# Kernel optimization log

Hardware: AMD Instinct MI355X
Metric: run time of the kernel (lower is better)

## Reference

```python
import jax, jax.numpy as jnp
import numpy as np

B, T, D, H = 8, 2048, 512, 128

def setup_inputs() -> dict:
    key = jax.random.key(0)
    ks = jax.random.split(key, 8)
    s = lambda fan_in: 1.0 / np.sqrt(fan_in)
    return {
        "x": jax.random.normal(ks[0], (B, T, D), jnp.float32),
        "prediction": jax.random.normal(ks[1], (B, T, D), jnp.float32),
        "Wq": jax.random.uniform(ks[2], (D, H), jnp.float32, -s(D), s(D)),
        "bq": jnp.zeros((H,), jnp.float32),
        "Wk": jax.random.uniform(ks[3], (D, H), jnp.float32, -s(D), s(D)),
        "bk": jnp.zeros((H,), jnp.float32),
        "Wv": jax.random.uniform(ks[4], (D, D), jnp.float32, -s(D), s(D)),
        "bv": jnp.zeros((D,), jnp.float32),
        "Wf": jax.random.uniform(ks[5], (2 * D, D), jnp.float32, -s(2 * D), s(2 * D)),
        "bf": jnp.zeros((D,), jnp.float32),
    }

def reference(x, prediction, Wq, bq, Wk, bk, Wv, bv, Wf, bf):
    # q,k: [B,T,H]; v: [B,T,D]
    q = jnp.einsum('btd,dh->bth', prediction, Wq) + bq
    k = jnp.einsum('btd,dh->bth', x, Wk) + bk
    v = jnp.einsum('btd,de->bte', x, Wv) + bv
    # unscaled attention scores [B,T,T]
    scores = jnp.einsum('bth,bsh->bts', q, k)
    attn = jax.nn.softmax(scores, axis=-1)
    attended = jnp.einsum('bts,bsd->btd', attn, v)
    fusion_input = jnp.concatenate([prediction, attended], axis=-1)  # [B,T,2D]
    return jax.nn.sigmoid(jnp.einsum('btf,fd->btd', fusion_input, Wf) + bf)
```

## Files before the change

### kernel.cpp

```cpp
#include <hip/hip_runtime.h>
#include <hip/hip_bf16.h>


#define APF_B 8
#define APF_T 2048
#define APF_D 512
#define APF_H 128
#define APF_M (APF_B * APF_T)
#define FA_SB 128

typedef unsigned short u16;
typedef __attribute__((ext_vector_type(8))) short short8;
typedef __attribute__((ext_vector_type(4))) float f32x4;
typedef __attribute__((ext_vector_type(16))) float f32x16;

static __device__ __forceinline__ u16 f2bf(float x) {
    union { float f; unsigned int u; } cv;
    cv.f = x;
    unsigned int u = cv.u + 0x7FFFu + ((cv.u >> 16) & 1u);
    return (u16)(u >> 16);
}

static __device__ __forceinline__ void load16_lds(const u16* g, u16* l) {
    __builtin_amdgcn_global_load_lds(
        (const __attribute__((address_space(1))) unsigned int*)g,
        (__attribute__((address_space(3))) unsigned int*)l,
        16, 0, 0);
}

static __device__ __forceinline__ f32x16 zero16() {
    f32x16 v;
#pragma unroll
    for (int i = 0; i < 16; ++i) v[i] = 0.f;
    return v;
}


__global__ __launch_bounds__(256) void cvt_pair(const float* __restrict__ in0,
                                                u16* __restrict__ out0,
                                                const float* __restrict__ in1,
                                                u16* __restrict__ out1, long n4)
{
    long i = blockIdx.x * 256L + threadIdx.x;
    const long stride = (long)gridDim.x * 256L;
    for (; i < 2 * n4; i += stride) {
        const float* in = (i < n4) ? in0 : in1;
        u16* out = (i < n4) ? out0 : out1;
        const long j = (i < n4) ? i : (i - n4);
        const float4 v = ((const float4*)in)[j];
        ushort4 o;
        o.x = f2bf(v.x); o.y = f2bf(v.y); o.z = f2bf(v.z); o.w = f2bf(v.w);
        ((ushort4*)out)[j] = o;
    }
}

__global__ __launch_bounds__(256) void prep_weights(
    const float* __restrict__ Wq, u16* __restrict__ WqT,
    const float* __restrict__ Wk, u16* __restrict__ WkT,
    const float* __restrict__ Wv, u16* __restrict__ WvT,
    const float* __restrict__ Wf, u16* __restrict__ WfT)
{
    const long e = blockIdx.x * 256L + threadIdx.x;
    if (e < 65536) {
        const long idx = e;
        const long n = idx / 512, k = idx % 512;
        WqT[idx] = f2bf(Wq[k * 128 + n]);
    } else if (e < 131072) {
        const long idx = e - 65536;
        const long n = idx / 512, k = idx % 512;
        WkT[idx] = f2bf(Wk[k * 128 + n]);
    } else if (e < 393216) {
        const long idx = e - 131072;
        const long n = idx / 512, k = idx % 512;
        WvT[idx] = f2bf(Wv[k * 512 + n]);
    } else if (e < 917504) {
        const long idx = e - 393216;
        const long n = idx / 1024, k = idx % 1024;
        WfT[idx] = f2bf(Wf[k * 512 + n]);
    }
}

template <int DUAL, int EPI, int BIASM, int VBLK>
__global__ __launch_bounds__(256) void mfma_gemm(
    const u16* __restrict__ Ap, const u16* __restrict__ A2p, long lda,
    const u16* __restrict__ Bp, const u16* __restrict__ Bp2, long ldb,
    const float* __restrict__ biasp, const float* __restrict__ bias2,
    void* __restrict__ Cp, void* __restrict__ Cp2, long ldc, int K,
    long sA, long sB, long sC)
{
    __shared__ u16 smA[128 * 32];
    __shared__ u16 smB[128 * 32];

    const int tid  = threadIdx.x;
    const int lane = tid & 63;
    const int wid  = tid >> 6;
    const int wr   = wid >> 1;
    const int wc   = wid & 1;

    const long row0 = (long)blockIdx.y * 128;
    const long col0 = (long)blockIdx.x * 128;
    const long z    = blockIdx.z;

    const u16* Abase = (DUAL == 2) ? (z ? A2p : Ap) : (Ap + z * sA);
    const u16* Bbase = (DUAL == 2) ? (z ? Bp2 : Bp) : (Bp + z * sB);

    f32x4 acc[4][4];
#pragma unroll
    for (int i = 0; i < 4; ++i)
#pragma unroll
        for (int j = 0; j < 4; ++j)
            acc[i][j] = (f32x4){0.f, 0.f, 0.f, 0.f};

    const int lrow = (lane >> 4) * 4;
    const int lcol = lane & 15;
    const int q8   = (lane >> 4) * 8;

    for (int kb = 0; kb < K; kb += 32) {
#pragma unroll
        for (int rep = 0; rep < 2; ++rep) {
            const int c  = tid + rep * 256;
            const int r  = c >> 2;
            const int kc = (c & 3) * 8;
            const int wbase = (wid * 64 + rep * 256) * 8;
            const u16* ga;
            if (DUAL == 1 && (kb + kc) >= APF_D) {
                ga = A2p + (row0 + r) * lda + (kb + kc - APF_D);
            } else {
                ga = Abase + (row0 + r) * lda + (kb + kc);
            }
            load16_lds(ga, &smA[wbase]);
            const u16* gb = Bbase + (col0 + r) * ldb + (kb + kc);
            load16_lds(gb, &smB[wbase]);
        }
        __syncthreads();

        short8 av[4], bv4[4];
#pragma unroll
        for (int ti = 0; ti < 4; ++ti)
            av[ti] = *(const short8*)&smA[(wr * 64 + ti * 16 + lcol) * 32 + q8];
#pragma unroll
        for (int tj = 0; tj < 4; ++tj)
            bv4[tj] = *(const short8*)&smB[(wc * 64 + tj * 16 + lcol) * 32 + q8];

#pragma unroll
        for (int ti = 0; ti < 4; ++ti)
#pragma unroll
            for (int tj = 0; tj < 4; ++tj)
                acc[ti][tj] = __builtin_amdgcn_mfma_f32_16x16x32_bf16(
                    av[ti], bv4[tj], acc[ti][tj], 0, 0, 0);
        __syncthreads();
    }

    const float* bias = (DUAL == 2 && z) ? bias2 : biasp;

#pragma unroll
    for (int ti = 0; ti < 4; ++ti) {
        const long m0t = row0 + wr * 64 + ti * 16 + lrow;
#pragma unroll
        for (int tj = 0; tj < 4; ++tj) {
            const long n = col0 + wc * 64 + tj * 16 + lcol;
            const float bn = (BIASM == 0 && bias != nullptr) ? bias[n] : 0.f;
            if (EPI == 0) {
                u16* C = (u16*)((DUAL == 2 && z) ? Cp2 : Cp) + ((DUAL == 2) ? 0 : z * sC);
#pragma unroll
                for (int r = 0; r < 4; ++r) {
                    const long m = m0t + r;
                    const float bm = (BIASM == 1) ? bias[m] : bn;
                    long idx;
                    if (VBLK) {
                        idx = ((((m >> 5) * 256) + (n >> 3)) << 8) +
                              ((m & 31) << 3) + (n & 7);
                    } else {
                        idx = m * ldc + n;
                    }
                    C[idx] = f2bf(acc[ti][tj][r] + bm);
                }
            } else {
                float* C = (float*)Cp;
#pragma unroll
                for (int r = 0; r < 4; ++r) {
                    const float val = acc[ti][tj][r] + bn;
                    C[(m0t + r) * ldc + n] = 1.0f / (1.0f + expf(-val));
                }
            }
        }
    }
}

__global__ __launch_bounds__(256, 2) void attn_fused(
    const u16* __restrict__ qg, const u16* __restrict__ kg,
    const u16* __restrict__ vTg, u16* __restrict__ attg)
{
    __shared__ u16 sQ[64 * 128];
    __shared__ u16 sK[128 * 128];
    __shared__ u16 sP[64 * 128];
    __shared__ float sRSp[256];

    const int tid  = threadIdx.x;
    const int lane = tid & 63;
    const int w    = tid >> 6;
    const int l31  = lane & 31;
    const int hi   = lane >> 5;

    const int  bid = blockIdx.x;
    const long z   = bid & 7;
    const int  r   = bid >> 3;
    const long q0  = (long)(r & 31) * 64;
    const long d0  = (long)(r >> 5) * 256;

    const u16* kbase0 = kg + z * (long)APF_T * APF_H;

    {
        const u16* qsrc = qg + (z * APF_T + q0) * APF_H;
#pragma unroll
        for (int rep = 0; rep < 4; ++rep) {
            const int c    = tid + rep * 256;
            const int row  = c >> 4;
            const int col8 = (c & 15) * 8;
            load16_lds(qsrc + row * APF_H + (col8 ^ ((row & 7) << 3)), &sQ[c * 8]);
        }
#pragma unroll
        for (int rep = 0; rep < 8; ++rep) {
            const int c    = tid + rep * 256;
            const int row  = c >> 4;
            const int col8 = (c & 15) * 8;
            load16_lds(kbase0 + row * APF_H + (col8 ^ ((row & 7) << 3)), &sK[c * 8]);
        }
    }
    __syncthreads();

    f32x16 oacc[2][2];
#pragma unroll
    for (int i = 0; i < 2; ++i)
#pragma unroll
        for (int j = 0; j < 2; ++j) oacc[i][j] = zero16();
    f32x16 rsacc[2];
    rsacc[0] = zero16(); rsacc[1] = zero16();

    const long dblk0 = (d0 >> 5) + w * 2;
    const u16* vzb = vTg + z * 1048576L + dblk0 * 65536L + (long)l31 * 8;

    const int pcol = w * 32 + l31;
    const int krow = w * 32 + l31;

    for (int kt = 0; kt < APF_T / FA_SB; ++kt) {
        f32x16 sacc[2];
        sacc[0] = zero16(); sacc[1] = zero16();
#pragma unroll
        for (int ks = 0; ks < 8; ++ks) {
            const int colk = ks * 16 + hi * 8;
            const short8 bv = *(const short8*)&sK[krow * 128 + (colk ^ ((krow & 7) << 3))];
#pragma unroll
            for (int qt = 0; qt < 2; ++qt) {
                const int qrow = qt * 32 + l31;
                const short8 av = *(const short8*)&sQ[qrow * 128 + (colk ^ ((qrow & 7) << 3))];
                sacc[qt] = __builtin_amdgcn_mfma_f32_32x32x16_bf16(av, bv, sacc[qt], 0, 0, 0);
            }
        }
        __syncthreads();

        if (kt + 1 < APF_T / FA_SB) {
            const u16* ksrc = kbase0 + (long)(kt + 1) * FA_SB * APF_H;
#pragma unroll
            for (int rep = 0; rep < 8; ++rep) {
                const int c    = tid + rep * 256;
                const int row  = c >> 4;
                const int col8 = (c & 15) * 8;
                load16_lds(ksrc + row * APF_H + (col8 ^ ((row & 7) << 3)), &sK[c * 8]);
            }
        }

        const long sbase = (long)kt * 16 + hi;
        short8 vf1[2][4];
#pragma unroll
        for (int dt = 0; dt < 2; ++dt)
#pragma unroll
            for (int ks = 0; ks < 4; ++ks)
                vf1[dt][ks] = *(const short8*)(vzb + dt * 65536L + (sbase + ks * 2) * 256);

#pragma unroll
        for (int qt = 0; qt < 2; ++qt)
#pragma unroll
            for (int rg = 0; rg < 16; ++rg) {
                const float e = __expf(sacc[qt][rg]);
                rsacc[qt][rg] += e;
                const int prow = qt * 32 + (rg & 3) + 8 * (rg >> 2) + 4 * hi;
                sP[prow * 128 + (pcol ^ ((prow & 7) << 3))] = f2bf(e);
            }
        __syncthreads();

#pragma unroll
        for (int ks = 0; ks < 4; ++ks) {
            const int colk = ks * 16 + hi * 8;
            short8 pa[2];
#pragma unroll
            for (int qt = 0; qt < 2; ++qt) {
                const int prow = qt * 32 + l31;
                pa[qt] = *(const short8*)&sP[prow * 128 + (colk ^ ((prow & 7) << 3))];
            }
#pragma unroll
            for (int dt = 0; dt < 2; ++dt)
#pragma unroll
                for (int qt = 0; qt < 2; ++qt)
                    oacc[qt][dt] = __builtin_amdgcn_mfma_f32_32x32x16_bf16(
                        pa[qt], vf1[dt][ks], oacc[qt][dt], 0, 0, 0);
        }

        short8 vf2[2][4];
#pragma unroll
        for (int dt = 0; dt < 2; ++dt)
#pragma unroll
            for (int ks = 0; ks < 4; ++ks)
                vf2[dt][ks] = *(const short8*)(vzb + dt * 65536L + (sbase + 8 + ks * 2) * 256);

#pragma unroll
        for (int ks = 0; ks < 4; ++ks) {
            const int colk = (ks + 4) * 16 + hi * 8;
            short8 pa[2];
#pragma unroll
            for (int qt = 0; qt < 2; ++qt) {
                const int prow = qt * 32 + l31;
                pa[qt] = *(const short8*)&sP[prow * 128 + (colk ^ ((prow & 7) << 3))];
            }
#pragma unroll
            for (int dt = 0; dt < 2; ++dt)
#pragma unroll
                for (int qt = 0; qt < 2; ++qt)
                    oacc[qt][dt] = __builtin_amdgcn_mfma_f32_32x32x16_bf16(
                        pa[qt], vf2[dt][ks], oacc[qt][dt], 0, 0, 0);
        }
    }

#pragma unroll
    for (int qt = 0; qt < 2; ++qt)
#pragma unroll
        for (int rg = 0; rg < 16; ++rg) {
            float s = rsacc[qt][rg];
            s += __shfl_xor(s, 1);
            s += __shfl_xor(s, 2);
            s += __shfl_xor(s, 4);
            s += __shfl_xor(s, 8);
            s += __shfl_xor(s, 16);
            rsacc[qt][rg] = s;
        }
    if (l31 == 0) {
#pragma unroll
        for (int qt = 0; qt < 2; ++qt)
#pragma unroll
            for (int rg = 0; rg < 16; ++rg) {
                const int row = qt * 32 + (rg & 3) + 8 * (rg >> 2) + 4 * hi;
                sRSp[w * 64 + row] = rsacc[qt][rg];
            }
    }
    __syncthreads();
    if (tid < 64) {
        const float t = sRSp[tid] + sRSp[64 + tid] + sRSp[128 + tid] + sRSp[192 + tid];
        sRSp[tid] = 1.0f / t;
    }
    __syncthreads();

    const long rowg0 = z * APF_T + q0;
    const long colg0 = d0 + (long)w * 64;
#pragma unroll
    for (int qt = 0; qt < 2; ++qt)
#pragma unroll
        for (int rg = 0; rg < 16; ++rg) {
            const int row = qt * 32 + (rg & 3) + 8 * (rg >> 2) + 4 * hi;
            const float inv = sRSp[row];
#pragma unroll
            for (int dt = 0; dt < 2; ++dt)
                attg[(rowg0 + row) * APF_D + colg0 + dt * 32 + l31] =
                    f2bf(oacc[qt][dt][rg] * inv);
        }
}

extern "C" void kernel_launch(void* const* d_in, const int* in_sizes, int n_in,
                              void* d_out, int out_size, void* d_ws, size_t ws_size,
                              hipStream_t stream)
{
    (void)in_sizes; (void)n_in; (void)out_size; (void)ws_size;

    const float* x    = (const float*)d_in[0];
    const float* pred = (const float*)d_in[1];
    const float* Wq   = (const float*)d_in[2];
    const float* bq   = (const float*)d_in[3];
    const float* Wk   = (const float*)d_in[4];
    const float* bk   = (const float*)d_in[5];
    const float* Wv   = (const float*)d_in[6];
    const float* bv   = (const float*)d_in[7];
    const float* Wf   = (const float*)d_in[8];
    const float* bfu  = (const float*)d_in[9];

    u16* wsp   = (u16*)d_ws;
    u16* xb    = wsp;
    u16* predb = xb    + (long)APF_M * APF_D;
    u16* qb    = predb + (long)APF_M * APF_D;
    u16* kbuf  = qb    + (long)APF_M * APF_H;
    u16* vTb   = kbuf  + (long)APF_M * APF_H;
    u16* attb  = vTb   + (long)APF_M * APF_D;
    u16* WqT   = attb  + (long)APF_M * APF_D;
    u16* WkT   = WqT   + (long)APF_H * APF_D;
    u16* WvT   = WkT   + (long)APF_H * APF_D;
    u16* WfT   = WvT   + (long)APF_D * APF_D;

    const dim3 thr(256);
    const long nBTD4 = (long)APF_M * APF_D / 4;

    cvt_pair<<<dim3(1024), thr, 0, stream>>>(x, xb, pred, predb, nBTD4);
    prep_weights<<<dim3(3584), thr, 0, stream>>>(Wq, WqT, Wk, WkT, Wv, WvT, Wf, WfT);

    mfma_gemm<2, 0, 0, 0><<<dim3(1, 128, 2), thr, 0, stream>>>(
        predb, xb, APF_D, WqT, WkT, APF_D, bq, bk, qb, kbuf, APF_H, APF_D,
        0, 0, 0);

    mfma_gemm<0, 0, 1, 1><<<dim3(16, 4, 8), thr, 0, stream>>>(
        WvT, nullptr, APF_D, xb, nullptr, APF_D, bv, nullptr, vTb, nullptr,
        APF_T, APF_D, 0, (long)APF_T * APF_D, (long)APF_D * APF_T);

    attn_fused<<<dim3(512), thr, 0, stream>>>(qb, kbuf, vTb, attb);

    mfma_gemm<1, 2, 0, 0><<<dim3(4, 128, 1), thr, 0, stream>>>(
        predb, attb, APF_D, WfT, nullptr, 2 * APF_D, bfu, nullptr, d_out, nullptr,
        APF_D, 2 * APF_D, 0, 0, 0);
}
```

Before: 270.2 us.

## Merge prep kernels, double-buffer GEMM LDS, shrink attention key block

Fuses the input conversion and weight transpose into a single launch to remove one kernel launch. Adds double-buffered LDS staging in the MFMA GEMM so the next K-tile loads while the current one computes. Reworks the attention kernel to use 64-key blocks with the four waves split across query and key halves, cutting LDS use so three blocks can fit per CU, at the cost of more iterations and barriers. The GEMM overlap relies on the barrier at the end of each iteration and on the async LDS loads for the next tile finishing before that tile is read.

```diff
diff --git a/kernel.cpp b/kernel.cpp
--- a/kernel.cpp
+++ b/kernel.cpp
@@ -7,7 +7,7 @@
 #define APF_D 512
 #define APF_H 128
 #define APF_M (APF_B * APF_T)
-#define FA_SB 128
+#define FA_SB 64
 
 typedef unsigned short u16;
 typedef __attribute__((ext_vector_type(8))) short short8;
@@ -36,47 +36,46 @@
 }
 
 
-__global__ __launch_bounds__(256) void cvt_pair(const float* __restrict__ in0,
-                                                u16* __restrict__ out0,
-                                                const float* __restrict__ in1,
-                                                u16* __restrict__ out1, long n4)
-{
-    long i = blockIdx.x * 256L + threadIdx.x;
-    const long stride = (long)gridDim.x * 256L;
-    for (; i < 2 * n4; i += stride) {
-        const float* in = (i < n4) ? in0 : in1;
-        u16* out = (i < n4) ? out0 : out1;
-        const long j = (i < n4) ? i : (i - n4);
-        const float4 v = ((const float4*)in)[j];
-        ushort4 o;
-        o.x = f2bf(v.x); o.y = f2bf(v.y); o.z = f2bf(v.z); o.w = f2bf(v.w);
-        ((ushort4*)out)[j] = o;
-    }
-}
-
-__global__ __launch_bounds__(256) void prep_weights(
+__global__ __launch_bounds__(256) void prep_all(
+    const float* __restrict__ x,    u16* __restrict__ xb,
+    const float* __restrict__ pred, u16* __restrict__ predb, long n4,
     const float* __restrict__ Wq, u16* __restrict__ WqT,
     const float* __restrict__ Wk, u16* __restrict__ WkT,
     const float* __restrict__ Wv, u16* __restrict__ WvT,
     const float* __restrict__ Wf, u16* __restrict__ WfT)
 {
-    const long e = blockIdx.x * 256L + threadIdx.x;
-    if (e < 65536) {
-        const long idx = e;
-        const long n = idx / 512, k = idx % 512;
-        WqT[idx] = f2bf(Wq[k * 128 + n]);
-    } else if (e < 131072) {
-        const long idx = e - 65536;
-        const long n = idx / 512, k = idx % 512;
-        WkT[idx] = f2bf(Wk[k * 128 + n]);
-    } else if (e < 393216) {
-        const long idx = e - 131072;
-        const long n = idx / 512, k = idx % 512;
-        WvT[idx] = f2bf(Wv[k * 512 + n]);
-    } else if (e < 917504) {
-        const long idx = e - 393216;
-        const long n = idx / 1024, k = idx % 1024;
-        WfT[idx] = f2bf(Wf[k * 512 + n]);
+    const int bid = blockIdx.x;
+    if (bid < 1024) {
+        long i = bid * 256L + threadIdx.x;
+        const long stride = 1024 * 256L;
+        for (; i < 2 * n4; i += stride) {
+            const float* in = (i < n4) ? x : pred;
+            u16* out = (i < n4) ? xb : predb;
+            const long j = (i < n4) ? i : (i - n4);
+            const float4 v = ((const float4*)in)[j];
+            ushort4 o;
+            o.x = f2bf(v.x); o.y = f2bf(v.y); o.z = f2bf(v.z); o.w = f2bf(v.w);
+            ((ushort4*)out)[j] = o;
+        }
+    } else {
+        const long e = (bid - 1024) * 256L + threadIdx.x;
+        if (e < 65536) {
+            const long idx = e;
+            const long n = idx / 512, k = idx % 512;
+            WqT[idx] = f2bf(Wq[k * 128 + n]);
+        } else if (e < 131072) {
+            const long idx = e - 65536;
+            const long n = idx / 512, k = idx % 512;
+            WkT[idx] = f2bf(Wk[k * 128 + n]);
+        } else if (e < 393216) {
+            const long idx = e - 131072;
+            const long n = idx / 512, k = idx % 512;
+            WvT[idx] = f2bf(Wv[k * 512 + n]);
+        } else if (e < 917504) {
+            const long idx = e - 393216;
+            const long n = idx / 1024, k = idx % 1024;
+            WfT[idx] = f2bf(Wf[k * 512 + n]);
+        }
     }
 }
 
@@ -88,8 +87,8 @@
     void* __restrict__ Cp, void* __restrict__ Cp2, long ldc, int K,
     long sA, long sB, long sC)
 {
-    __shared__ u16 smA[128 * 32];
-    __shared__ u16 smB[128 * 32];
+    __shared__ u16 smA[2][128 * 32];
+    __shared__ u16 smB[2][128 * 32];
 
     const int tid  = threadIdx.x;
     const int lane = tid & 63;
@@ -115,7 +114,7 @@
     const int lcol = lane & 15;
     const int q8   = (lane >> 4) * 8;
 
-    for (int kb = 0; kb < K; kb += 32) {
+    auto stage = [&](int buf, int kb) {
 #pragma unroll
         for (int rep = 0; rep < 2; ++rep) {
             const int c  = tid + rep * 256;
@@ -128,19 +127,27 @@
             } else {
                 ga = Abase + (row0 + r) * lda + (kb + kc);
             }
-            load16_lds(ga, &smA[wbase]);
+            load16_lds(ga, &smA[buf][wbase]);
             const u16* gb = Bbase + (col0 + r) * ldb + (kb + kc);
-            load16_lds(gb, &smB[wbase]);
-        }
-        __syncthreads();
+            load16_lds(gb, &smB[buf][wbase]);
+        }
+    };
+
+    const int NT = K / 32;
+    stage(0, 0);
+    __syncthreads();
+    int cur = 0;
+
+    for (int t = 0; t < NT; ++t) {
+        if (t + 1 < NT) stage(cur ^ 1, (t + 1) * 32);
 
         short8 av[4], bv4[4];
 #pragma unroll
         for (int ti = 0; ti < 4; ++ti)
-            av[ti] = *(const short8*)&smA[(wr * 64 + ti * 16 + lcol) * 32 + q8];
+            av[ti] = *(const short8*)&smA[cur][(wr * 64 + ti * 16 + lcol) * 32 + q8];
 #pragma unroll
         for (int tj = 0; tj < 4; ++tj)
-            bv4[tj] = *(const short8*)&smB[(wc * 64 + tj * 16 + lcol) * 32 + q8];
+            bv4[tj] = *(const short8*)&smB[cur][(wc * 64 + tj * 16 + lcol) * 32 + q8];
 
 #pragma unroll
         for (int ti = 0; ti < 4; ++ti)
@@ -148,7 +155,9 @@
             for (int tj = 0; tj < 4; ++tj)
                 acc[ti][tj] = __builtin_amdgcn_mfma_f32_16x16x32_bf16(
                     av[ti], bv4[tj], acc[ti][tj], 0, 0, 0);
+
         __syncthreads();
+        cur ^= 1;
     }
 
     const float* bias = (DUAL == 2 && z) ? bias2 : biasp;
@@ -187,20 +196,22 @@
     }
 }
 
-__global__ __launch_bounds__(256, 2) void attn_fused(
+__global__ __launch_bounds__(256, 3) void attn_fused(
     const u16* __restrict__ qg, const u16* __restrict__ kg,
     const u16* __restrict__ vTg, u16* __restrict__ attg)
 {
     __shared__ u16 sQ[64 * 128];
-    __shared__ u16 sK[128 * 128];
-    __shared__ u16 sP[64 * 128];
-    __shared__ float sRSp[256];
+    __shared__ u16 sK[64 * 128];
+    __shared__ u16 sP[64 * 64];
+    __shared__ float sRS[192];
 
     const int tid  = threadIdx.x;
     const int lane = tid & 63;
     const int w    = tid >> 6;
     const int l31  = lane & 31;
     const int hi   = lane >> 5;
+    const int qb   = w >> 1;
+    const int sb   = w & 1;
 
     const int  bid = blockIdx.x;
     const long z   = bid & 7;
@@ -217,14 +228,14 @@
             const int c    = tid + rep * 256;
             const int row  = c >> 4;
             const int col8 = (c & 15) * 8;
-            load16_lds(qsrc + row * APF_H + (col8 ^ ((row & 7) << 3)), &sQ[c * 8]);
-        }
-#pragma unroll
-        for (int rep = 0; rep < 8; ++rep) {
+            load16_lds(qsrc + row * APF_H + (col8 ^ ((row & 15) << 3)), &sQ[c * 8]);
+        }
+#pragma unroll
+        for (int rep = 0; rep < 4; ++rep) {
             const int c    = tid + rep * 256;
             const int row  = c >> 4;
             const int col8 = (c & 15) * 8;
-            load16_lds(kbase0 + row * APF_H + (col8 ^ ((row & 7) << 3)), &sK[c * 8]);
+            load16_lds(kbase0 + row * APF_H + (col8 ^ ((row & 15) << 3)), &sK[c * 8]);
         }
     }
     __syncthreads();
@@ -234,69 +245,62 @@
     for (int i = 0; i < 2; ++i)
 #pragma unroll
         for (int j = 0; j < 2; ++j) oacc[i][j] = zero16();
-    f32x16 rsacc[2];
-    rsacc[0] = zero16(); rsacc[1] = zero16();
+    f32x16 rsacc = zero16();
 
     const long dblk0 = (d0 >> 5) + w * 2;
     const u16* vzb = vTg + z * 1048576L + dblk0 * 65536L + (long)l31 * 8;
 
-    const int pcol = w * 32 + l31;
-    const int krow = w * 32 + l31;
+    const int qrow = qb * 32 + l31;
+    const int krow = sb * 32 + l31;
+    const int pcol = sb * 32 + l31;
 
     for (int kt = 0; kt < APF_T / FA_SB; ++kt) {
-        f32x16 sacc[2];
-        sacc[0] = zero16(); sacc[1] = zero16();
+        f32x16 sacc = zero16();
 #pragma unroll
         for (int ks = 0; ks < 8; ++ks) {
             const int colk = ks * 16 + hi * 8;
-            const short8 bv = *(const short8*)&sK[krow * 128 + (colk ^ ((krow & 7) << 3))];
-#pragma unroll
-            for (int qt = 0; qt < 2; ++qt) {
-                const int qrow = qt * 32 + l31;
-                const short8 av = *(const short8*)&sQ[qrow * 128 + (colk ^ ((qrow & 7) << 3))];
-                sacc[qt] = __builtin_amdgcn_mfma_f32_32x32x16_bf16(av, bv, sacc[qt], 0, 0, 0);
-            }
+            const short8 av = *(const short8*)&sQ[qrow * 128 + (colk ^ ((qrow & 15) << 3))];
+            const short8 bv = *(const short8*)&sK[krow * 128 + (colk ^ ((krow & 15) << 3))];
+            sacc = __builtin_amdgcn_mfma_f32_32x32x16_bf16(av, bv, sacc, 0, 0, 0);
         }
         __syncthreads();
 
         if (kt + 1 < APF_T / FA_SB) {
             const u16* ksrc = kbase0 + (long)(kt + 1) * FA_SB * APF_H;
 #pragma unroll
-            for (int rep = 0; rep < 8; ++rep) {
+            for (int rep = 0; rep < 4; ++rep) {
                 const int c    = tid + rep * 256;
                 const int row  = c >> 4;
                 const int col8 = (c & 15) * 8;
-                load16_lds(ksrc + row * APF_H + (col8 ^ ((row & 7) << 3)), &sK[c * 8]);
+                load16_lds(ksrc + row * APF_H + (col8 ^ ((row & 15) << 3)), &sK[c * 8]);
             }
         }
 
-        const long sbase = (long)kt * 16 + hi;
-        short8 vf1[2][4];
+        const long sbase = (long)kt * 8 + hi;
+        short8 vf1[2][2];
 #pragma unroll
         for (int dt = 0; dt < 2; ++dt)
 #pragma unroll
-            for (int ks = 0; ks < 4; ++ks)
+            for (int ks = 0; ks < 2; ++ks)
                 vf1[dt][ks] = *(const short8*)(vzb + dt * 65536L + (sbase + ks * 2) * 256);
 
 #pragma unroll
-        for (int qt = 0; qt < 2; ++qt)
-#pragma unroll
-            for (int rg = 0; rg < 16; ++rg) {
-                const float e = __expf(sacc[qt][rg]);
-                rsacc[qt][rg] += e;
-                const int prow = qt * 32 + (rg & 3) + 8 * (rg >> 2) + 4 * hi;
-                sP[prow * 128 + (pcol ^ ((prow & 7) << 3))] = f2bf(e);
-            }
+        for (int rg = 0; rg < 16; ++rg) {
+            const float e = __expf(sacc[rg]);
+            rsacc[rg] += e;
+            const int prow = qb * 32 + (rg & 3) + 8 * (rg >> 2) + 4 * hi;
+            sP[prow * 64 + (pcol ^ ((prow & 7) << 3))] = f2bf(e);
+        }
         __syncthreads();
 
 #pragma unroll
-        for (int ks = 0; ks < 4; ++ks) {
+        for (int ks = 0; ks < 2; ++ks) {
             const int colk = ks * 16 + hi * 8;
             short8 pa[2];
 #pragma unroll
             for (int qt = 0; qt < 2; ++qt) {
                 const int prow = qt * 32 + l31;
-                pa[qt] = *(const short8*)&sP[prow * 128 + (colk ^ ((prow & 7) << 3))];
+                pa[qt] = *(const short8*)&sP[prow * 64 + (colk ^ ((prow & 7) << 3))];
             }
 #pragma unroll
             for (int dt = 0; dt < 2; ++dt)
@@ -306,21 +310,21 @@
                         pa[qt], vf1[dt][ks], oacc[qt][dt], 0, 0, 0);
         }
 
-        short8 vf2[2][4];
+        short8 vf2[2][2];
 #pragma unroll
         for (int dt = 0; dt < 2; ++dt)
 #pragma unroll
-            for (int ks = 0; ks < 4; ++ks)
-                vf2[dt][ks] = *(const short8*)(vzb + dt * 65536L + (sbase + 8 + ks * 2) * 256);
-
-#pragma unroll
-        for (int ks = 0; ks < 4; ++ks) {
-            const int colk = (ks + 4) * 16 + hi * 8;
+            for (int ks = 0; ks < 2; ++ks)
+                vf2[dt][ks] = *(const short8*)(vzb + dt * 65536L + (sbase + (ks + 2) * 2) * 256);
+
+#pragma unroll
+        for (int ks = 0; ks < 2; ++ks) {
+            const int colk = (ks + 2) * 16 + hi * 8;
             short8 pa[2];
 #pragma unroll
             for (int qt = 0; qt < 2; ++qt) {
                 const int prow = qt * 32 + l31;
-                pa[qt] = *(const short8*)&sP[prow * 128 + (colk ^ ((prow & 7) << 3))];
+                pa[qt] = *(const short8*)&sP[prow * 64 + (colk ^ ((prow & 7) << 3))];
             }
 #pragma unroll
             for (int dt = 0; dt < 2; ++dt)
@@ -332,30 +336,27 @@
     }
 
 #pragma unroll
-    for (int qt = 0; qt < 2; ++qt)
+    for (int rg = 0; rg < 16; ++rg) {
+        float s = rsacc[rg];
+        s += __shfl_xor(s, 1);
+        s += __shfl_xor(s, 2);
+        s += __shfl_xor(s, 4);
+        s += __shfl_xor(s, 8);
+        s += __shfl_xor(s, 16);
+        rsacc[rg] = s;
+    }
+    if (l31 == 0) {
 #pragma unroll
         for (int rg = 0; rg < 16; ++rg) {
-            float s = rsacc[qt][rg];
-            s += __shfl_xor(s, 1);
-            s += __shfl_xor(s, 2);
-            s += __shfl_xor(s, 4);
-            s += __shfl_xor(s, 8);
-            s += __shfl_xor(s, 16);
-            rsacc[qt][rg] = s;
-        }
-    if (l31 == 0) {
-#pragma unroll
-        for (int qt = 0; qt < 2; ++qt)
-#pragma unroll
-            for (int rg = 0; rg < 16; ++rg) {
-                const int row = qt * 32 + (rg & 3) + 8 * (rg >> 2) + 4 * hi;
-                sRSp[w * 64 + row] = rsacc[qt][rg];
-            }
+            const int row = (rg & 3) + 8 * (rg >> 2) + 4 * hi;
+            sRS[w * 32 + row] = rsacc[rg];
+        }
     }
     __syncthreads();
     if (tid < 64) {
-        const float t = sRSp[tid] + sRSp[64 + tid] + sRSp[128 + tid] + sRSp[192 + tid];
-        sRSp[tid] = 1.0f / t;
+        const int qb2 = tid >> 5, r2 = tid & 31;
+        sRS[128 + tid] = 1.0f / (sRS[(qb2 * 2 + 0) * 32 + r2] +
+                                 sRS[(qb2 * 2 + 1) * 32 + r2]);
     }
     __syncthreads();
 
@@ -366,7 +367,7 @@
 #pragma unroll
         for (int rg = 0; rg < 16; ++rg) {
             const int row = qt * 32 + (rg & 3) + 8 * (rg >> 2) + 4 * hi;
-            const float inv = sRSp[row];
+            const float inv = sRS[128 + row];
 #pragma unroll
             for (int dt = 0; dt < 2; ++dt)
                 attg[(rowg0 + row) * APF_D + colg0 + dt * 32 + l31] =
@@ -406,8 +407,8 @@
     const dim3 thr(256);
     const long nBTD4 = (long)APF_M * APF_D / 4;
 
-    cvt_pair<<<dim3(1024), thr, 0, stream>>>(x, xb, pred, predb, nBTD4);
-    prep_weights<<<dim3(3584), thr, 0, stream>>>(Wq, WqT, Wk, WkT, Wv, WvT, Wf, WfT);
+    prep_all<<<dim3(1024 + 3584), thr, 0, stream>>>(
+        x, xb, pred, predb, nBTD4, Wq, WqT, Wk, WkT, Wv, WvT, Wf, WfT);
 
     mfma_gemm<2, 0, 0, 0><<<dim3(1, 128, 2), thr, 0, stream>>>(
         predb, xb, APF_D, WqT, WkT, APF_D, bq, bk, qb, kbuf, APF_H, APF_D,
```

Result: faster. 262.7 us (-2.8%).
